# Kernel tuning notes

Measured on AMD Instinct MI355X. Metric: run time of the kernel, lower is better.

## Reference

```python
import jax, jax.numpy as jnp
import numpy as np

B, S, K, N, GROUP = 4, 8, 4096, 11008, 128
NUM_GROUPS = K // GROUP  # 32


def setup_inputs() -> dict:
    key = jax.random.key(0)
    k1, k2, k3 = jax.random.split(key, 3)
    x = jax.random.normal(k1, (B, S, K), dtype=jnp.float16)
    # packed int4 weights: each byte holds two nibbles (low nibble = even k, high = odd k)
    weight_packed = jax.random.randint(k2, (N, K // 2), 0, 256, dtype=jnp.int32)
    # scales: abs(randn)*0.1 in fp16, as in the torch module
    scales = (jnp.abs(jax.random.normal(k3, (N, NUM_GROUPS), dtype=jnp.float16)) * jnp.float16(0.1))
    return {"x": x, "weight_packed": weight_packed, "scales": scales}


def _dequant(weight_packed, scales, Kd):
    # unpack: low nibble -> even index k, high nibble -> odd index k+1
    n = weight_packed.shape[0]
    low = weight_packed & 0xF
    high = (weight_packed >> 4) & 0xF
    w = jnp.stack([low, high], axis=-1).reshape(n, Kd)  # [N, K] int in [0,16)
    g = Kd // scales.shape[1]
    # group-wise dequant: scale * (w - 8), scale applied in fp32 (matches fp32-accum kernel)
    wq = (w.astype(jnp.float32) - 8.0).reshape(n, scales.shape[1], g)
    wdeq = wq * scales.astype(jnp.float32)[:, :, None]
    return wdeq.reshape(n, Kd)  # [N, K] fp32


def reference(x, weight_packed, scales):
    b, s, kd = x.shape
    wdeq = _dequant(weight_packed, scales, kd)           # [N, K]
    x2 = x.reshape(-1, kd).astype(jnp.float32)           # [M, K], fp32 accumulation
    out = jnp.einsum('mk,nk->mn', x2, wdeq)              # [M, N]
    return out.astype(jnp.float16).reshape(b, s, -1)
```

## Files before the change

kernel.cpp:

```cpp
#include <hip/hip_runtime.h>

#define M 32
#define N 11008
#define K 4096
#define NGROUPS 32
#define BN 16
#define KSPLIT 4
#define KRANGE (K / KSPLIT)
#define BK 256
#define NCHUNK (KRANGE / BK)

typedef _Float16 half8 __attribute__((ext_vector_type(8)));
typedef _Float16 half4 __attribute__((ext_vector_type(4)));
typedef float floatx4 __attribute__((ext_vector_type(4)));

#define WPAIR 260
#define XPAIR 520

__device__ inline void gll16(const void* g, void* l) {
    __builtin_amdgcn_global_load_lds(
        (const __attribute__((address_space(1))) unsigned int*)g,
        (__attribute__((address_space(3))) unsigned int*)l, 16, 0, 0);
}

__global__ __launch_bounds__(512) void xcvt_kernel(
    const float* __restrict__ x, _Float16* __restrict__ xf)
{
    int i = (blockIdx.x * 512 + threadIdx.x) * 4;
    float4 v = *(const float4*)(x + i);
    half4 h;
    h[0] = (_Float16)v.x; h[1] = (_Float16)v.y;
    h[2] = (_Float16)v.z; h[3] = (_Float16)v.w;
    *(half4*)(xf + i) = h;
}

__global__ __launch_bounds__(256) void int4_gemm_kernel(
    const _Float16* __restrict__ xf,
    const int* __restrict__ wp,
    const float* __restrict__ scales,
    float* __restrict__ out)
{
    __shared__ int wsh[8 * WPAIR];
    __shared__ _Float16 xs[16 * XPAIR];

    const int t    = threadIdx.x;
    const int lane = t & 63;
    const int w    = t >> 6;
    const int n0   = blockIdx.x * BN;
    const int ks   = blockIdx.y;
    const int row  = lane & 15;
    const int quad = lane >> 4;

    floatx4 acc0 = {0.f, 0.f, 0.f, 0.f};
    floatx4 acc1 = {0.f, 0.f, 0.f, 0.f};

    const half8 c1032 = (half8)(_Float16)1032.0f;

    for (int c = 0; c < NCHUNK; ++c) {
        const int kc = ks * KRANGE + c * BK;

        #pragma unroll
        for (int i = 0; i < 2; ++i) {
            int p = w * 2 + i;
            int r = 2 * p + (lane >> 5);
            const int* g = wp + (long)(n0 + r) * (K / 2) + (kc >> 1) + (lane & 31) * 4;
            gll16(g, &wsh[p * WPAIR]);
        }
        #pragma unroll
        for (int i = 0; i < 4; ++i) {
            int p = w * 4 + i;
            int m = 2 * p + (lane >> 5);
            const _Float16* g = xf + m * K + kc + (lane & 31) * 8;
            gll16(g, &xs[p * XPAIR]);
        }
        __syncthreads();

        const float s = scales[(n0 + row) * NGROUPS + (kc >> 7) + (w >> 1)];
        floatx4 t0 = {0.f, 0.f, 0.f, 0.f};
        floatx4 t1 = {0.f, 0.f, 0.f, 0.f};
        #pragma unroll
        for (int kk = 0; kk < 2; ++kk) {
            const int kl = w * 64 + kk * 32;
            int4 wv = *(const int4*)&wsh[(row >> 1) * WPAIR + (row & 1) * 128 + (kl >> 1) + quad * 4];
            uint4 uw;
            {
                unsigned int b;
                b = (unsigned int)wv.x;
                uw.x = ((b | (b << 12)) & 0x000F000Fu) | 0x64006400u;
                b = (unsigned int)wv.y;
                uw.y = ((b | (b << 12)) & 0x000F000Fu) | 0x64006400u;
                b = (unsigned int)wv.z;
                uw.z = ((b | (b << 12)) & 0x000F000Fu) | 0x64006400u;
                b = (unsigned int)wv.w;
                uw.w = ((b | (b << 12)) & 0x000F000Fu) | 0x64006400u;
            }
            half8 bfrag = __builtin_bit_cast(half8, uw) - c1032;

            int x0 = (row >> 1) * XPAIR + (row & 1) * 256 + kl + quad * 8;
            half8 a0 = *(const half8*)&xs[x0];
            half8 a1 = *(const half8*)&xs[x0 + 8 * XPAIR];
            t0 = __builtin_amdgcn_mfma_f32_16x16x32_f16(a0, bfrag, t0, 0, 0, 0);
            t1 = __builtin_amdgcn_mfma_f32_16x16x32_f16(a1, bfrag, t1, 0, 0, 0);
        }
        #pragma unroll
        for (int r = 0; r < 4; ++r) {
            acc0[r] += s * t0[r];
            acc1[r] += s * t1[r];
        }
        __syncthreads();
    }

    float* red = (float*)xs;
    #pragma unroll
    for (int r = 0; r < 4; ++r) {
        red[w * 512 + (quad * 4 + r) * 16 + row]      = acc0[r];
        red[w * 512 + (quad * 4 + r + 16) * 16 + row] = acc1[r];
    }
    __syncthreads();
    #pragma unroll
    for (int i = 0; i < 2; ++i) {
        int o = t + 256 * i;
        float sum = red[o] + red[512 + o] + red[1024 + o] + red[1536 + o];
        int m = o >> 4;
        int n = o & 15;
        atomicAdd(&out[m * N + n0 + n], sum);
    }
}

extern "C" void kernel_launch(void* const* d_in, const int* in_sizes, int n_in,
                              void* d_out, int out_size, void* d_ws, size_t ws_size,
                              hipStream_t stream) {
    const float* x      = (const float*)d_in[0];
    const int* wp       = (const int*)d_in[1];
    const float* scales = (const float*)d_in[2];
    float* out          = (float*)d_out;
    _Float16* xf16      = (_Float16*)d_ws;

    hipMemsetAsync(out, 0, (size_t)M * N * sizeof(float), stream);
    xcvt_kernel<<<dim3((M * K) / (512 * 4)), 512, 0, stream>>>(x, xf16);
    int4_gemm_kernel<<<dim3(N / BN, KSPLIT), 256, 0, stream>>>(xf16, wp, scales, out);
}
```

Before: 141.8 us.

## Restructure int4 GEMM to single-chunk blocks with partial buffers and reduction kernel

```diff
diff --git a/kernel.cpp b/kernel.cpp
--- a/kernel.cpp
+++ b/kernel.cpp
@@ -4,11 +4,10 @@
 #define N 11008
 #define K 4096
 #define NGROUPS 32
-#define BN 16
-#define KSPLIT 4
+#define BN 64
+#define KSPLIT 16
 #define KRANGE (K / KSPLIT)
-#define BK 256
-#define NCHUNK (KRANGE / BK)
+#define MN (M * N)
 
 typedef _Float16 half8 __attribute__((ext_vector_type(8)));
 typedef _Float16 half4 __attribute__((ext_vector_type(4)));
@@ -38,9 +37,9 @@
     const _Float16* __restrict__ xf,
     const int* __restrict__ wp,
     const float* __restrict__ scales,
-    float* __restrict__ out)
+    float* __restrict__ part)
 {
-    __shared__ int wsh[8 * WPAIR];
+    __shared__ int wsh[32 * WPAIR];
     __shared__ _Float16 xs[16 * XPAIR];
 
     const int t    = threadIdx.x;
@@ -51,80 +50,81 @@
     const int row  = lane & 15;
     const int quad = lane >> 4;
 
+    const int nw = n0 + w * 16 + row;
+    const float s0 = scales[nw * NGROUPS + ks * 2];
+    const float s1 = scales[nw * NGROUPS + ks * 2 + 1];
+
+    #pragma unroll
+    for (int i = 0; i < 8; ++i) {
+        int p = w * 8 + i;
+        int r = 2 * p + (lane >> 5);
+        const int* g = wp + (long)(n0 + r) * (K / 2) + ks * (KRANGE / 2) + (lane & 31) * 4;
+        gll16(g, &wsh[p * WPAIR]);
+    }
+    #pragma unroll
+    for (int i = 0; i < 4; ++i) {
+        int p = w * 4 + i;
+        int m = 2 * p + (lane >> 5);
+        const _Float16* g = xf + m * K + ks * KRANGE + (lane & 31) * 8;
+        gll16(g, &xs[p * XPAIR]);
+    }
+    __syncthreads();
+
+    const half8 c1032 = (half8)(_Float16)1032.0f;
     floatx4 acc0 = {0.f, 0.f, 0.f, 0.f};
     floatx4 acc1 = {0.f, 0.f, 0.f, 0.f};
 
-    const half8 c1032 = (half8)(_Float16)1032.0f;
+    const int wr    = w * 16 + row;
+    const int wbase = (wr >> 1) * WPAIR + (wr & 1) * 128 + quad * 4;
+    const int xbase = (row >> 1) * XPAIR + (row & 1) * 256 + quad * 8;
 
-    for (int c = 0; c < NCHUNK; ++c) {
-        const int kc = ks * KRANGE + c * BK;
-
-        #pragma unroll
-        for (int i = 0; i < 2; ++i) {
-            int p = w * 2 + i;
-            int r = 2 * p + (lane >> 5);
-            const int* g = wp + (long)(n0 + r) * (K / 2) + (kc >> 1) + (lane & 31) * 4;
-            gll16(g, &wsh[p * WPAIR]);
-        }
-        #pragma unroll
-        for (int i = 0; i < 4; ++i) {
-            int p = w * 4 + i;
-            int m = 2 * p + (lane >> 5);
-            const _Float16* g = xf + m * K + kc + (lane & 31) * 8;
-            gll16(g, &xs[p * XPAIR]);
-        }
-        __syncthreads();
-
-        const float s = scales[(n0 + row) * NGROUPS + (kc >> 7) + (w >> 1)];
+    #pragma unroll
+    for (int g = 0; g < 2; ++g) {
         floatx4 t0 = {0.f, 0.f, 0.f, 0.f};
         floatx4 t1 = {0.f, 0.f, 0.f, 0.f};
         #pragma unroll
-        for (int kk = 0; kk < 2; ++kk) {
-            const int kl = w * 64 + kk * 32;
-            int4 wv = *(const int4*)&wsh[(row >> 1) * WPAIR + (row & 1) * 128 + (kl >> 1) + quad * 4];
+        for (int kk = 0; kk < 4; ++kk) {
+            const int kq = g * 4 + kk;
+            int4 wv = *(const int4*)&wsh[wbase + kq * 16];
             uint4 uw;
             {
                 unsigned int b;
-                b = (unsigned int)wv.x;
-                uw.x = ((b | (b << 12)) & 0x000F000Fu) | 0x64006400u;
-                b = (unsigned int)wv.y;
-                uw.y = ((b | (b << 12)) & 0x000F000Fu) | 0x64006400u;
-                b = (unsigned int)wv.z;
-                uw.z = ((b | (b << 12)) & 0x000F000Fu) | 0x64006400u;
-                b = (unsigned int)wv.w;
-                uw.w = ((b | (b << 12)) & 0x000F000Fu) | 0x64006400u;
+                b = (unsigned int)wv.x; uw.x = ((b | (b << 12)) & 0x000F000Fu) | 0x64006400u;
+                b = (unsigned int)wv.y; uw.y = ((b | (b << 12)) & 0x000F000Fu) | 0x64006400u;
+                b = (unsigned int)wv.z; uw.z = ((b | (b << 12)) & 0x000F000Fu) | 0x64006400u;
+                b = (unsigned int)wv.w; uw.w = ((b | (b << 12)) & 0x000F000Fu) | 0x64006400u;
             }
             half8 bfrag = __builtin_bit_cast(half8, uw) - c1032;
-
-            int x0 = (row >> 1) * XPAIR + (row & 1) * 256 + kl + quad * 8;
-            half8 a0 = *(const half8*)&xs[x0];
-            half8 a1 = *(const half8*)&xs[x0 + 8 * XPAIR];
+            half8 a0 = *(const half8*)&xs[xbase + kq * 32];
+            half8 a1 = *(const half8*)&xs[xbase + 8 * XPAIR + kq * 32];
             t0 = __builtin_amdgcn_mfma_f32_16x16x32_f16(a0, bfrag, t0, 0, 0, 0);
             t1 = __builtin_amdgcn_mfma_f32_16x16x32_f16(a1, bfrag, t1, 0, 0, 0);
         }
+        const float s = g ? s1 : s0;
         #pragma unroll
         for (int r = 0; r < 4; ++r) {
             acc0[r] += s * t0[r];
             acc1[r] += s * t1[r];
         }
-        __syncthreads();
     }
 
-    float* red = (float*)xs;
+    float* po = part + (long)ks * MN;
     #pragma unroll
     for (int r = 0; r < 4; ++r) {
-        red[w * 512 + (quad * 4 + r) * 16 + row]      = acc0[r];
-        red[w * 512 + (quad * 4 + r + 16) * 16 + row] = acc1[r];
+        int mr = quad * 4 + r;
+        po[mr * N + nw]        = acc0[r];
+        po[(mr + 16) * N + nw] = acc1[r];
     }
-    __syncthreads();
+}
+
+__global__ __launch_bounds__(256) void reduce_kernel(
+    const float* __restrict__ part, float* __restrict__ out)
+{
+    int o = blockIdx.x * 256 + threadIdx.x;
+    float s = 0.f;
     #pragma unroll
-    for (int i = 0; i < 2; ++i) {
-        int o = t + 256 * i;
-        float sum = red[o] + red[512 + o] + red[1024 + o] + red[1536 + o];
-        int m = o >> 4;
-        int n = o & 15;
-        atomicAdd(&out[m * N + n0 + n], sum);
-    }
+    for (int j = 0; j < KSPLIT; ++j) s += part[(long)j * MN + o];
+    out[o] = s;
 }
 
 extern "C" void kernel_launch(void* const* d_in, const int* in_sizes, int n_in,
@@ -134,9 +134,11 @@
     const int* wp       = (const int*)d_in[1];
     const float* scales = (const float*)d_in[2];
     float* out          = (float*)d_out;
-    _Float16* xf16      = (_Float16*)d_ws;
 
-    hipMemsetAsync(out, 0, (size_t)M * N * sizeof(float), stream);
+    _Float16* xf16 = (_Float16*)d_ws;
+    float* part    = (float*)((char*)d_ws + (size_t)M * K * 2);
+
     xcvt_kernel<<<dim3((M * K) / (512 * 4)), 512, 0, stream>>>(x, xf16);
-    int4_gemm_kernel<<<dim3(N / BN, KSPLIT), 256, 0, stream>>>(xf16, wp, scales, out);
+    int4_gemm_kernel<<<dim3(N / BN, KSPLIT), 256, 0, stream>>>(xf16, wp, scales, part);
+    reduce_kernel<<<dim3(MN / 256), 256, 0, stream>>>(part, out);
 }
```

New measurement: 145.7 us. +2.8%, slower.

## Load x fragments directly from global memory and drop x LDS staging

Applied to the files above, without the earlier changes.

```diff
diff --git a/kernel.cpp b/kernel.cpp
--- a/kernel.cpp
+++ b/kernel.cpp
@@ -4,18 +4,17 @@
 #define N 11008
 #define K 4096
 #define NGROUPS 32
-#define BN 16
 #define KSPLIT 4
 #define KRANGE (K / KSPLIT)
 #define BK 256
 #define NCHUNK (KRANGE / BK)
+#define MN (M * N)
 
 typedef _Float16 half8 __attribute__((ext_vector_type(8)));
 typedef _Float16 half4 __attribute__((ext_vector_type(4)));
 typedef float floatx4 __attribute__((ext_vector_type(4)));
 
 #define WPAIR 260
-#define XPAIR 520
 
 __device__ inline void gll16(const void* g, void* l) {
     __builtin_amdgcn_global_load_lds(
@@ -34,73 +33,66 @@
     *(half4*)(xf + i) = h;
 }
 
-__global__ __launch_bounds__(256) void int4_gemm_kernel(
+__global__ __launch_bounds__(256, 8) void int4_gemm_kernel(
     const _Float16* __restrict__ xf,
     const int* __restrict__ wp,
     const float* __restrict__ scales,
     float* __restrict__ out)
 {
     __shared__ int wsh[8 * WPAIR];
-    __shared__ _Float16 xs[16 * XPAIR];
 
     const int t    = threadIdx.x;
     const int lane = t & 63;
     const int w    = t >> 6;
-    const int n0   = blockIdx.x * BN;
+    const int n0   = blockIdx.x * 16;
     const int ks   = blockIdx.y;
     const int row  = lane & 15;
     const int quad = lane >> 4;
+    const int nw   = n0 + row;
 
+    const half8 c1032 = (half8)(_Float16)1032.0f;
     floatx4 acc0 = {0.f, 0.f, 0.f, 0.f};
     floatx4 acc1 = {0.f, 0.f, 0.f, 0.f};
 
-    const half8 c1032 = (half8)(_Float16)1032.0f;
-
     for (int c = 0; c < NCHUNK; ++c) {
-        const int kc = ks * KRANGE + c * BK;
+        const int k0 = ks * KRANGE + c * BK;
 
         #pragma unroll
         for (int i = 0; i < 2; ++i) {
             int p = w * 2 + i;
             int r = 2 * p + (lane >> 5);
-            const int* g = wp + (long)(n0 + r) * (K / 2) + (kc >> 1) + (lane & 31) * 4;
+            const int* g = wp + (long)(n0 + r) * (K / 2) + (k0 >> 1) + (lane & 31) * 4;
             gll16(g, &wsh[p * WPAIR]);
-        }
-        #pragma unroll
-        for (int i = 0; i < 4; ++i) {
-            int p = w * 4 + i;
-            int m = 2 * p + (lane >> 5);
-            const _Float16* g = xf + m * K + kc + (lane & 31) * 8;
-            gll16(g, &xs[p * XPAIR]);
         }
         __syncthreads();
 
-        const float s = scales[(n0 + row) * NGROUPS + (kc >> 7) + (w >> 1)];
+        const int kw = k0 + w * 64;
+        half8 a[2][2];
+        #pragma unroll
+        for (int kk = 0; kk < 2; ++kk)
+            #pragma unroll
+            for (int i = 0; i < 2; ++i)
+                a[kk][i] = *(const half8*)(xf + (i * 16 + row) * K + kw + kk * 32 + quad * 8);
+
+        const float s = scales[nw * NGROUPS + (k0 >> 7) + (w >> 1)];
+
         floatx4 t0 = {0.f, 0.f, 0.f, 0.f};
         floatx4 t1 = {0.f, 0.f, 0.f, 0.f};
         #pragma unroll
         for (int kk = 0; kk < 2; ++kk) {
-            const int kl = w * 64 + kk * 32;
-            int4 wv = *(const int4*)&wsh[(row >> 1) * WPAIR + (row & 1) * 128 + (kl >> 1) + quad * 4];
+            int4 wv = *(const int4*)&wsh[(row >> 1) * WPAIR + (row & 1) * 128
+                                         + w * 32 + kk * 16 + quad * 4];
             uint4 uw;
             {
                 unsigned int b;
-                b = (unsigned int)wv.x;
-                uw.x = ((b | (b << 12)) & 0x000F000Fu) | 0x64006400u;
-                b = (unsigned int)wv.y;
-                uw.y = ((b | (b << 12)) & 0x000F000Fu) | 0x64006400u;
-                b = (unsigned int)wv.z;
-                uw.z = ((b | (b << 12)) & 0x000F000Fu) | 0x64006400u;
-                b = (unsigned int)wv.w;
-                uw.w = ((b | (b << 12)) & 0x000F000Fu) | 0x64006400u;
+                b = (unsigned int)wv.x; uw.x = ((b | (b << 12)) & 0x000F000Fu) | 0x64006400u;
+                b = (unsigned int)wv.y; uw.y = ((b | (b << 12)) & 0x000F000Fu) | 0x64006400u;
+                b = (unsigned int)wv.z; uw.z = ((b | (b << 12)) & 0x000F000Fu) | 0x64006400u;
+                b = (unsigned int)wv.w; uw.w = ((b | (b << 12)) & 0x000F000Fu) | 0x64006400u;
             }
             half8 bfrag = __builtin_bit_cast(half8, uw) - c1032;
-
-            int x0 = (row >> 1) * XPAIR + (row & 1) * 256 + kl + quad * 8;
-            half8 a0 = *(const half8*)&xs[x0];
-            half8 a1 = *(const half8*)&xs[x0 + 8 * XPAIR];
-            t0 = __builtin_amdgcn_mfma_f32_16x16x32_f16(a0, bfrag, t0, 0, 0, 0);
-            t1 = __builtin_amdgcn_mfma_f32_16x16x32_f16(a1, bfrag, t1, 0, 0, 0);
+            t0 = __builtin_amdgcn_mfma_f32_16x16x32_f16(a[kk][0], bfrag, t0, 0, 0, 0);
+            t1 = __builtin_amdgcn_mfma_f32_16x16x32_f16(a[kk][1], bfrag, t1, 0, 0, 0);
         }
         #pragma unroll
         for (int r = 0; r < 4; ++r) {
@@ -110,7 +102,7 @@
         __syncthreads();
     }
 
-    float* red = (float*)xs;
+    float* red = (float*)wsh;
     #pragma unroll
     for (int r = 0; r < 4; ++r) {
         red[w * 512 + (quad * 4 + r) * 16 + row]      = acc0[r];
@@ -136,7 +128,7 @@
     float* out          = (float*)d_out;
     _Float16* xf16      = (_Float16*)d_ws;
 
-    hipMemsetAsync(out, 0, (size_t)M * N * sizeof(float), stream);
+    hipMemsetAsync(out, 0, (size_t)MN * sizeof(float), stream);
     xcvt_kernel<<<dim3((M * K) / (512 * 4)), 512, 0, stream>>>(x, xf16);
-    int4_gemm_kernel<<<dim3(N / BN, KSPLIT), 256, 0, stream>>>(xf16, wp, scales, out);
+    int4_gemm_kernel<<<dim3(N / 16, KSPLIT), 256, 0, stream>>>(xf16, wp, scales, out);
 }
```

After: 149.8 us. +5.6%, slower.
